# Performance work log

Hardware: AMD Instinct MI355X
Metric: run time of the kernel (lower is better)

The kernel has to match this reference:

```python
import jax, jax.numpy as jnp
import numpy as np

E, V, F_, B = 8192, 2048, 2048, 8
H, DEC, EDGE, META = 128, 128, 2, 4
MEMH, MEMAGG, AGGH = 256, 128, 128
IN_DIM = DEC + EDGE + META  # 134


def _incidence(idx, n):
    # dense (n, E) 0/1 incidence matrix, as used by torch.mm in the original
    return jnp.zeros((n, idx.shape[0]), jnp.float32).at[idx, jnp.arange(idx.shape[0])].set(1.0)


def setup_inputs() -> dict:
    key = jax.random.key(0)
    ks = jax.random.split(key, 32)
    var_idx = jax.random.randint(ks[0], (E,), 0, V)          # variable of each edge
    fun_idx = jax.random.randint(ks[1], (E,), 0, F_)         # clause of each edge
    batch_of_var = jax.random.randint(ks[2], (V,), 0, B)     # problem id of each variable
    variable_mask = _incidence(var_idx, V)                   # (V, E)
    function_mask = _incidence(fun_idx, F_)                  # (F, E)
    b_variable_mask = jnp.zeros((V, B), jnp.float32).at[jnp.arange(V), batch_of_var].set(1.0)

    def lin(k, i, o):
        kw, kb = jax.random.split(k)
        return (jax.random.normal(kw, (i, o), jnp.float32) * 0.05,
                jax.random.normal(kb, (o,), jnp.float32) * 0.05)

    p = {}
    for pre, k0 in (("v", 10), ("f", 20)):
        p[pre + "M1w"], p[pre + "M1b"] = lin(ks[k0], IN_DIM, MEMH)
        p[pre + "M2w"], p[pre + "M2b"] = lin(ks[k0 + 1], MEMH, MEMAGG)
        p[pre + "A1w"], p[pre + "A1b"] = lin(ks[k0 + 2], MEMAGG + EDGE, AGGH)
        p[pre + "A2w"], p[pre + "A2b"] = lin(ks[k0 + 3], AGGH, H)

    return dict(
        variable_state=jax.random.normal(ks[3], (E, H), jnp.float32),
        function_state=jax.random.normal(ks[4], (E, H), jnp.float32),
        decimator_variable_state=jax.random.normal(ks[5], (E, DEC), jnp.float32),
        decimator_function_state=jax.random.normal(ks[6], (E, DEC), jnp.float32),
        edge_feature=jax.random.normal(ks[7], (E, EDGE), jnp.float32),
        meta_data=jax.random.normal(ks[8], (B, META), jnp.float32),
        active_mask=jax.random.randint(ks[9], (B, 1), 0, 2),
        variable_mask=variable_mask, variable_mask_t=variable_mask.T,
        function_mask=function_mask, function_mask_t=function_mask.T,
        b_variable_mask=b_variable_mask,
        **p,
    )


def _aggregate(state, feature, mask, mask_t, W1, b1, W2, b2, A1, c1, A2, c2):
    # MessageAggregator (include_self_message=False, edge_mask=None)
    h = jax.nn.relu(state @ W1 + b1)       # (E, MEMH)  pre-aggregation transform
    h = h @ W2 + b2                        # (E, MEMAGG)
    agg = mask_t @ (mask @ h) - h          # node-sum broadcast back to edges, minus self message
    a = jax.nn.relu(jnp.concatenate([agg, feature], 1) @ A1 + c1)  # post-agg transform
    return a @ A2 + c2                     # (E, H)


def reference(variable_state, function_state, decimator_variable_state,
              decimator_function_state, edge_feature, meta_data, active_mask,
              variable_mask, variable_mask_t, function_mask, function_mask_t,
              b_variable_mask,
              vM1w, vM1b, vM2w, vM2b, vA1w, vA1b, vA2w, vA2b,
              fM1w, fM1b, fM2w, fM2b, fA1w, fA1b, fA2w, fA2b):
    # active mask broadcast: batch -> variables -> edges (dense mm chain as in torch)
    mask = variable_mask_t @ (b_variable_mask @ active_mask.astype(jnp.float32))  # (E, 1)
    # meta-data broadcast: batch -> variables -> edges
    graph_feat = variable_mask_t @ (b_variable_mask @ meta_data)                  # (E, META)

    dvs = jnp.concatenate([decimator_variable_state, edge_feature, graph_feat], 1)
    agg_v = _aggregate(dvs, edge_feature, variable_mask, variable_mask_t,
                       vM1w, vM1b, vM2w, vM2b, vA1w, vA1b, vA2w, vA2b)
    function_state = mask * agg_v + (1.0 - mask) * function_state  # dropout: identity (eval)

    dfs = jnp.concatenate([decimator_function_state, edge_feature, graph_feat], 1)
    agg_f = _aggregate(dfs, edge_feature, function_mask, function_mask_t,
                       fM1w, fM1b, fM2w, fM2b, fA1w, fA1b, fA2w, fA2b)
    variable_state = mask * agg_f + (1.0 - mask) * variable_state

    return (variable_state, function_state)
```

## Files before the change

kernel.cpp:

```cpp
#include <hip/hip_runtime.h>

#define E_N 8192
#define V_N 2048
#define F_N 2048
#define B_N 8
#define H_N 128
#define DEC_N 128
#define EDGE_N 2
#define META_N 4
#define IN_DIM 134
#define MEMH 256
#define MEMAGG 128
#define AGGH 128

typedef __attribute__((ext_vector_type(8))) short short8;
typedef __attribute__((ext_vector_type(4))) float f32x4;

__device__ inline unsigned short f2bf(float x) {
    unsigned u = __float_as_uint(x);
    unsigned r = (u + 0x7FFFu + ((u >> 16) & 1u)) >> 16;
    return (unsigned short)r;
}

__device__ inline short8 pack8(float4 u0, float4 u1) {
    short8 s;
    s[0] = (short)f2bf(u0.x); s[1] = (short)f2bf(u0.y);
    s[2] = (short)f2bf(u0.z); s[3] = (short)f2bf(u0.w);
    s[4] = (short)f2bf(u1.x); s[5] = (short)f2bf(u1.y);
    s[6] = (short)f2bf(u1.z); s[7] = (short)f2bf(u1.w);
    return s;
}

struct RDesc { const float* src; unsigned short* dst; int K; int N; int Kp; };
struct SetupArgs { RDesc d[8]; float* nszero; const float* bvm; int* bov; };

__global__ __launch_bounds__(256) void k_setup(SetupArgs p) {
    if (blockIdx.y == 8) {
        if (blockIdx.x < 8) {
            int v = blockIdx.x * 256 + threadIdx.x;
            float s = 0.f;
#pragma unroll
            for (int b = 0; b < B_N; ++b) s += p.bvm[v * B_N + b] * (float)b;
            p.bov[v] = (int)(s + 0.5f);
        }
        return;
    }
    int gid = (int)((blockIdx.y * 160 + blockIdx.x) * 256 + threadIdx.x);
    const int NZ4 = (V_N + F_N) * MEMAGG / 4;
    if (gid < NZ4) ((float4*)p.nszero)[gid] = (float4){0.f, 0.f, 0.f, 0.f};

    RDesc d = p.d[blockIdx.y];
    int i = blockIdx.x * 256 + threadIdx.x;
    int total = d.Kp * d.N;
    if (i >= total) return;
    int elem = i & 7;
    int lane = (i >> 3) & 63;
    int f    = i >> 9;
    int c16n = d.N >> 4;
    int c16 = f % c16n, kc = f / c16n;
    int k = kc * 32 + (lane >> 4) * 8 + elem;
    int c = c16 * 16 + (lane & 15);
    float v = (k < d.K) ? d.src[(size_t)k * d.N + c] : 0.f;
    d.dst[i] = f2bf(v);
}

__global__ __launch_bounds__(256) void k_idx(const float* __restrict__ vmt,
                                             const float* __restrict__ fmt,
                                             int* __restrict__ vidx,
                                             int* __restrict__ fidx,
                                             const int* __restrict__ bov,
                                             const int* __restrict__ active,
                                             const float* __restrict__ meta,
                                             float* __restrict__ emask,
                                             float* __restrict__ gfeat) {
    int wave = (int)((blockIdx.x * blockDim.x + threadIdx.x) >> 6);
    int lane = threadIdx.x & 63;
    bool isVar = wave < E_N;
    const float* m = isVar ? vmt : fmt;
    int* out = isVar ? vidx : fidx;
    int e = isVar ? wave : wave - E_N;
    const float4* row = (const float4*)(m + (size_t)e * V_N);

    int pos = -1;
#pragma unroll
    for (int half = 0; half < 2; ++half) {
        if (pos < 0) {
            float4 v0 = row[half * 256 + lane];
            float4 v1 = row[half * 256 + 64 + lane];
            float4 v2 = row[half * 256 + 128 + lane];
            float4 v3 = row[half * 256 + 192 + lane];
            int hit = -1;
            float4 vv[4] = {v0, v1, v2, v3};
#pragma unroll
            for (int j = 0; j < 4; ++j) {
                float4 v = vv[j];
                int c = (half * 256 + j * 64 + lane) * 4;
                if (hit < 0) {
                    if      (v.x != 0.f) hit = c;
                    else if (v.y != 0.f) hit = c + 1;
                    else if (v.z != 0.f) hit = c + 2;
                    else if (v.w != 0.f) hit = c + 3;
                }
            }
            unsigned long long bm = __ballot(hit >= 0);
            if (bm) pos = __shfl(hit, __ffsll((long long)bm) - 1);
        }
    }
    if (lane == 0) {
        out[e] = pos;
        if (isVar) {
            int b = bov[pos];
            emask[e] = (float)active[b];
            ((float4*)gfeat)[e] = ((const float4*)meta)[b];
        }
    }
}

struct F1Args {
    const float* dec[2];
    const float* ef;
    const float* gfeat;
    const unsigned short* wpack[2];
    const float* b1[2];
    const float* b2[2];
    const int* idx[2];
    float* h2[2];
    float* ns[2];
};

__global__ __launch_bounds__(256) void k_fused1(F1Args A) {
    int br = blockIdx.y;
    const float* dec = A.dec[br];
    const unsigned short* W1f = A.wpack[br];
    const unsigned short* W2f = A.wpack[br] + 160 * 256;
    const float* b1 = A.b1[br];
    const float* b2 = A.b2[br];
    const int* idx = A.idx[br];
    float* h2o = A.h2[br];
    float* ns  = A.ns[br];

    int tid = threadIdx.x;
    int wave = tid >> 6, lane = tid & 63;
    int lrow = lane & 15, lgrp = lane >> 4;
    int e0 = blockIdx.x * 16;

    __shared__ unsigned short h1s[16 * 256];

    int n0 = wave * 64;
    f32x4 acc1[4];
#pragma unroll
    for (int nt = 0; nt < 4; ++nt) {
        float bv = b1[n0 + nt * 16 + lrow];
        acc1[nt] = (f32x4){bv, bv, bv, bv};
    }
    const float4* dec4 = (const float4*)dec;
    int r = e0 + lrow;
#pragma unroll
    for (int kc = 0; kc < 5; ++kc) {
        short8 a;
        if (kc < 4) {
            float4 u0 = dec4[(size_t)r * 32 + kc * 8 + lgrp * 2];
            float4 u1 = dec4[(size_t)r * 32 + kc * 8 + lgrp * 2 + 1];
            a = pack8(u0, u1);
        } else {
            short8 z = (short8)0;
            if (lgrp == 0) {
                z[0] = (short)f2bf(A.ef[r * 2]);
                z[1] = (short)f2bf(A.ef[r * 2 + 1]);
                z[2] = (short)f2bf(A.gfeat[r * 4]);
                z[3] = (short)f2bf(A.gfeat[r * 4 + 1]);
                z[4] = (short)f2bf(A.gfeat[r * 4 + 2]);
                z[5] = (short)f2bf(A.gfeat[r * 4 + 3]);
            }
            a = z;
        }
#pragma unroll
        for (int nt = 0; nt < 4; ++nt) {
            short8 b = *(const short8*)(W1f + ((size_t)(kc * 16 + (n0 >> 4) + nt) * 64 + lane) * 8);
            acc1[nt] = __builtin_amdgcn_mfma_f32_16x16x32_bf16(a, b, acc1[nt], 0, 0, 0);
        }
    }
#pragma unroll
    for (int nt = 0; nt < 4; ++nt)
#pragma unroll
        for (int j = 0; j < 4; ++j) {
            int row = lgrp * 4 + j;
            int col = n0 + nt * 16 + lrow;
            h1s[row * 256 + (col ^ ((row & 7) << 3))] = f2bf(fmaxf(acc1[nt][j], 0.f));
        }
    __syncthreads();

    int c0 = wave * 32;
    f32x4 acc2[2];
#pragma unroll
    for (int nt = 0; nt < 2; ++nt) {
        float bv = b2[c0 + nt * 16 + lrow];
        acc2[nt] = (f32x4){bv, bv, bv, bv};
    }
#pragma unroll
    for (int kc = 0; kc < 8; ++kc) {
        int kb = kc * 32 + lgrp * 8;
        short8 a2 = *(const short8*)(h1s + lrow * 256 + (kb ^ ((lrow & 7) << 3)));
#pragma unroll
        for (int nt = 0; nt < 2; ++nt) {
            short8 b = *(const short8*)(W2f + ((size_t)(kc * 8 + (c0 >> 4) + nt) * 64 + lane) * 8);
            acc2[nt] = __builtin_amdgcn_mfma_f32_16x16x32_bf16(a2, b, acc2[nt], 0, 0, 0);
        }
    }
#pragma unroll
    for (int j = 0; j < 4; ++j) {
        int row = e0 + lgrp * 4 + j;
        int node = idx[row];
#pragma unroll
        for (int nt = 0; nt < 2; ++nt) {
            int col = c0 + nt * 16 + lrow;
            float v = acc2[nt][j];
            h2o[(size_t)row * 128 + col] = v;
            atomicAdd(ns + (size_t)node * 128 + col, v);
        }
    }
}

struct F2Args {
    const unsigned short* wpack[2];
    const float* c1[2];
    const float* c2[2];
    const float* h2[2];
    const float* ns[2];
    const int* idx[2];
    const float* ef;
    const float* emask;
    const float* oldst[2];
    float* outst[2];
};

__global__ __launch_bounds__(256) void k_fused2(F2Args A) {
    int br = blockIdx.y;
    const unsigned short* A1f = A.wpack[br] + 160 * 256 + 256 * 128;
    const unsigned short* A2f = A1f + 160 * 128;
    const float* c1 = A.c1[br];
    const float* c2 = A.c2[br];
    const float* h2 = A.h2[br];
    const float* ns = A.ns[br];
    const int* idx = A.idx[br];
    const float* oldst = A.oldst[br];
    float* outst = A.outst[br];

    int tid = threadIdx.x;
    int wave = tid >> 6, lane = tid & 63;
    int lrow = lane & 15, lgrp = lane >> 4;
    int e0 = blockIdx.x * 16;

    __shared__ unsigned short as_[16 * 128];

    int n0 = wave * 32;
    f32x4 accp[2];
#pragma unroll
    for (int nt = 0; nt < 2; ++nt) {
        float bv = c1[n0 + nt * 16 + lrow];
        accp[nt] = (f32x4){bv, bv, bv, bv};
    }
    const float4* ns4 = (const float4*)ns;
    const float4* h24 = (const float4*)h2;
    int r = e0 + lrow;
    int node = idx[r];
#pragma unroll
    for (int kc = 0; kc < 5; ++kc) {
        short8 a;
        if (kc < 4) {
            float4 u0 = ns4[(size_t)node * 32 + kc * 8 + lgrp * 2];
            float4 u1 = ns4[(size_t)node * 32 + kc * 8 + lgrp * 2 + 1];
            float4 v0 = h24[(size_t)r * 32 + kc * 8 + lgrp * 2];
            float4 v1 = h24[(size_t)r * 32 + kc * 8 + lgrp * 2 + 1];
            float4 d0 = {u0.x - v0.x, u0.y - v0.y, u0.z - v0.z, u0.w - v0.w};
            float4 d1 = {u1.x - v1.x, u1.y - v1.y, u1.z - v1.z, u1.w - v1.w};
            a = pack8(d0, d1);
        } else {
            short8 z = (short8)0;
            if (lgrp == 0) {
                z[0] = (short)f2bf(A.ef[r * 2]);
                z[1] = (short)f2bf(A.ef[r * 2 + 1]);
            }
            a = z;
        }
#pragma unroll
        for (int nt = 0; nt < 2; ++nt) {
            short8 b = *(const short8*)(A1f + ((size_t)(kc * 8 + (n0 >> 4) + nt) * 64 + lane) * 8);
            accp[nt] = __builtin_amdgcn_mfma_f32_16x16x32_bf16(a, b, accp[nt], 0, 0, 0);
        }
    }
#pragma unroll
    for (int nt = 0; nt < 2; ++nt)
#pragma unroll
        for (int j = 0; j < 4; ++j) {
            int row = lgrp * 4 + j;
            int col = n0 + nt * 16 + lrow;
            as_[row * 128 + (col ^ ((row & 7) << 3))] = f2bf(fmaxf(accp[nt][j], 0.f));
        }
    __syncthreads();

    f32x4 acco[2];
#pragma unroll
    for (int nt = 0; nt < 2; ++nt) {
        float bv = c2[n0 + nt * 16 + lrow];
        acco[nt] = (f32x4){bv, bv, bv, bv};
    }
#pragma unroll
    for (int kc = 0; kc < 4; ++kc) {
        int kb = kc * 32 + lgrp * 8;
        short8 a2 = *(const short8*)(as_ + lrow * 128 + (kb ^ ((lrow & 7) << 3)));
#pragma unroll
        for (int nt = 0; nt < 2; ++nt) {
            short8 b = *(const short8*)(A2f + ((size_t)(kc * 8 + (n0 >> 4) + nt) * 64 + lane) * 8);
            acco[nt] = __builtin_amdgcn_mfma_f32_16x16x32_bf16(a2, b, acco[nt], 0, 0, 0);
        }
    }
#pragma unroll
    for (int j = 0; j < 4; ++j) {
        int row = e0 + lgrp * 4 + j;
        float m = A.emask[row];
#pragma unroll
        for (int nt = 0; nt < 2; ++nt) {
            int col = n0 + nt * 16 + lrow;
            float old = oldst[(size_t)row * 128 + col];
            outst[(size_t)row * 128 + col] = m * acco[nt][j] + (1.f - m) * old;
        }
    }
}

extern "C" void kernel_launch(void* const* d_in, const int* in_sizes, int n_in,
                              void* d_out, int out_size, void* d_ws, size_t ws_size,
                              hipStream_t stream) {
    const float* variable_state = (const float*)d_in[0];
    const float* function_state = (const float*)d_in[1];
    const float* dec_v          = (const float*)d_in[2];
    const float* dec_f          = (const float*)d_in[3];
    const float* ef             = (const float*)d_in[4];
    const float* meta           = (const float*)d_in[5];
    const int*   active         = (const int*)d_in[6];
    const float* vmask_t        = (const float*)d_in[8];
    const float* fmask_t        = (const float*)d_in[10];
    const float* bvm            = (const float*)d_in[11];
    const float* vM1w = (const float*)d_in[12]; const float* vM1b = (const float*)d_in[13];
    const float* vM2w = (const float*)d_in[14]; const float* vM2b = (const float*)d_in[15];
    const float* vA1w = (const float*)d_in[16]; const float* vA1b = (const float*)d_in[17];
    const float* vA2w = (const float*)d_in[18]; const float* vA2b = (const float*)d_in[19];
    const float* fM1w = (const float*)d_in[20]; const float* fM1b = (const float*)d_in[21];
    const float* fM2w = (const float*)d_in[22]; const float* fM2b = (const float*)d_in[23];
    const float* fA1w = (const float*)d_in[24]; const float* fA1b = (const float*)d_in[25];
    const float* fA2w = (const float*)d_in[26]; const float* fA2b = (const float*)d_in[27];

    float* out_vs = (float*)d_out;
    float* out_fs = (float*)d_out + (size_t)E_N * H_N;

    int*   var_idx = (int*)d_ws;
    int*   fun_idx = var_idx + E_N;
    int*   bov     = fun_idx + E_N;
    float* emask   = (float*)(bov + V_N);
    float* gfeat   = emask + E_N;
    float* hv2     = gfeat + (size_t)E_N * 4;
    float* hf2     = hv2 + (size_t)E_N * MEMAGG;
    float* nsv     = hf2 + (size_t)E_N * MEMAGG;
    float* nsf     = nsv + (size_t)V_N * MEMAGG;
    unsigned short* wpack = (unsigned short*)(nsf + (size_t)F_N * MEMAGG);
    const int PBR = 160 * 256 + 256 * 128 + 160 * 128 + 128 * 128;
    unsigned short* wpv = wpack;
    unsigned short* wpf = wpack + PBR;

    SetupArgs sp;
    sp.d[0] = {vM1w, wpv,                          IN_DIM, MEMH,   160};
    sp.d[1] = {vM2w, wpv + 160 * 256,              MEMH,   MEMAGG, 256};
    sp.d[2] = {vA1w, wpv + 160 * 256 + 256 * 128,  130,    AGGH,   160};
    sp.d[3] = {vA2w, wpv + 160 * 256 + 256 * 128 + 160 * 128, 128, H_N, 128};
    sp.d[4] = {fM1w, wpf,                          IN_DIM, MEMH,   160};
    sp.d[5] = {fM2w, wpf + 160 * 256,              MEMH,   MEMAGG, 256};
    sp.d[6] = {fA1w, wpf + 160 * 256 + 256 * 128,  130,    AGGH,   160};
    sp.d[7] = {fA2w, wpf + 160 * 256 + 256 * 128 + 160 * 128, 128, H_N, 128};
    sp.nszero = nsv;
    sp.bvm = bvm;
    sp.bov = bov;
    k_setup<<<dim3(160, 9), 256, 0, stream>>>(sp);

    k_idx<<<(2 * E_N) / 4, 256, 0, stream>>>(vmask_t, fmask_t, var_idx, fun_idx,
                                             bov, active, meta, emask, gfeat);

    F1Args f1;
    f1.dec[0] = dec_v;  f1.dec[1] = dec_f;
    f1.ef = ef;         f1.gfeat = gfeat;
    f1.wpack[0] = wpv;  f1.wpack[1] = wpf;
    f1.b1[0] = vM1b;    f1.b1[1] = fM1b;
    f1.b2[0] = vM2b;    f1.b2[1] = fM2b;
    f1.idx[0] = var_idx; f1.idx[1] = fun_idx;
    f1.h2[0] = hv2;     f1.h2[1] = hf2;
    f1.ns[0] = nsv;     f1.ns[1] = nsf;
    k_fused1<<<dim3(E_N / 16, 2), 256, 0, stream>>>(f1);

    F2Args f2;
    f2.wpack[0] = wpv;  f2.wpack[1] = wpf;
    f2.c1[0] = vA1b;    f2.c1[1] = fA1b;
    f2.c2[0] = vA2b;    f2.c2[1] = fA2b;
    f2.h2[0] = hv2;     f2.h2[1] = hf2;
    f2.ns[0] = nsv;     f2.ns[1] = nsf;
    f2.idx[0] = var_idx; f2.idx[1] = fun_idx;
    f2.ef = ef;         f2.emask = emask;
    f2.oldst[0] = function_state;  f2.oldst[1] = variable_state;
    f2.outst[0] = out_fs;          f2.outst[1] = out_vs;
    k_fused2<<<dim3(E_N / 16, 2), 256, 0, stream>>>(f2);
}
```

Measured before the change: 58.37 us.

## Fuse function-mask index scan into first fused kernel and batch row scans per wave

The incidence-row scan for the function branch moves out of the standalone index kernel and into the start of the first fused MLP kernel. Found indices go to shared memory for the scatter-add and are also written to global for the later kernel. The variable-branch scan now gives each wave four rows with all first-half loads issued up front to raise memory-level parallelism. The aim is to overlap the function-mask scan with variable-side work and shorten the index kernel, at the cost of extra latency and register pressure at the start of the fused kernel.

```diff
diff --git a/kernel.cpp b/kernel.cpp
--- a/kernel.cpp
+++ b/kernel.cpp
@@ -29,6 +29,16 @@
     s[4] = (short)f2bf(u1.x); s[5] = (short)f2bf(u1.y);
     s[6] = (short)f2bf(u1.z); s[7] = (short)f2bf(u1.w);
     return s;
+}
+
+__device__ inline int probe4(float4 v, int c, int hit) {
+    if (hit < 0) {
+        if      (v.x != 0.f) hit = c;
+        else if (v.y != 0.f) hit = c + 1;
+        else if (v.z != 0.f) hit = c + 2;
+        else if (v.w != 0.f) hit = c + 3;
+    }
+    return hit;
 }
 
 struct RDesc { const float* src; unsigned short* dst; int K; int N; int Kp; };
@@ -64,54 +74,43 @@
     d.dst[i] = f2bf(v);
 }
 
-__global__ __launch_bounds__(256) void k_idx(const float* __restrict__ vmt,
-                                             const float* __restrict__ fmt,
-                                             int* __restrict__ vidx,
-                                             int* __restrict__ fidx,
-                                             const int* __restrict__ bov,
-                                             const int* __restrict__ active,
-                                             const float* __restrict__ meta,
-                                             float* __restrict__ emask,
-                                             float* __restrict__ gfeat) {
-    int wave = (int)((blockIdx.x * blockDim.x + threadIdx.x) >> 6);
-    int lane = threadIdx.x & 63;
-    bool isVar = wave < E_N;
-    const float* m = isVar ? vmt : fmt;
-    int* out = isVar ? vidx : fidx;
-    int e = isVar ? wave : wave - E_N;
-    const float4* row = (const float4*)(m + (size_t)e * V_N);
-
-    int pos = -1;
-#pragma unroll
-    for (int half = 0; half < 2; ++half) {
-        if (pos < 0) {
-            float4 v0 = row[half * 256 + lane];
-            float4 v1 = row[half * 256 + 64 + lane];
-            float4 v2 = row[half * 256 + 128 + lane];
-            float4 v3 = row[half * 256 + 192 + lane];
-            int hit = -1;
-            float4 vv[4] = {v0, v1, v2, v3};
+__global__ __launch_bounds__(256) void k_scanv(const float* __restrict__ vmt,
+                                               int* __restrict__ vidx,
+                                               const int* __restrict__ bov,
+                                               const int* __restrict__ active,
+                                               const float* __restrict__ meta,
+                                               float* __restrict__ emask,
+                                               float* __restrict__ gfeat) {
+    int wave = threadIdx.x >> 6, lane = threadIdx.x & 63;
+    int e0 = blockIdx.x * 16 + wave * 4;
+    const float4* rp[4];
+    float4 h[4][4];
+#pragma unroll
+    for (int r = 0; r < 4; ++r) {
+        rp[r] = (const float4*)(vmt + (size_t)(e0 + r) * V_N);
+#pragma unroll
+        for (int j = 0; j < 4; ++j) h[r][j] = rp[r][j * 64 + lane];
+    }
+#pragma unroll
+    for (int r = 0; r < 4; ++r) {
+        int hit = -1;
+#pragma unroll
+        for (int j = 0; j < 4; ++j) hit = probe4(h[r][j], (j * 64 + lane) * 4, hit);
+        unsigned long long bm = __ballot(hit >= 0);
+        if (!bm) {
 #pragma unroll
             for (int j = 0; j < 4; ++j) {
-                float4 v = vv[j];
-                int c = (half * 256 + j * 64 + lane) * 4;
-                if (hit < 0) {
-                    if      (v.x != 0.f) hit = c;
-                    else if (v.y != 0.f) hit = c + 1;
-                    else if (v.z != 0.f) hit = c + 2;
-                    else if (v.w != 0.f) hit = c + 3;
-                }
+                float4 v = rp[r][256 + j * 64 + lane];
+                hit = probe4(v, 1024 + (j * 64 + lane) * 4, hit);
             }
-            unsigned long long bm = __ballot(hit >= 0);
-            if (bm) pos = __shfl(hit, __ffsll((long long)bm) - 1);
-        }
-    }
-    if (lane == 0) {
-        out[e] = pos;
-        if (isVar) {
+            bm = __ballot(hit >= 0);
+        }
+        int pos = __shfl(hit, __ffsll((long long)bm) - 1);
+        if (lane == 0) {
+            vidx[e0 + r] = pos;
             int b = bov[pos];
-            emask[e] = (float)active[b];
-            ((float4*)gfeat)[e] = ((const float4*)meta)[b];
+            emask[e0 + r] = (float)active[b];
+            ((float4*)gfeat)[e0 + r] = ((const float4*)meta)[b];
         }
     }
 }
@@ -120,10 +119,11 @@
     const float* dec[2];
     const float* ef;
     const float* gfeat;
+    const float* fmt;
     const unsigned short* wpack[2];
     const float* b1[2];
     const float* b2[2];
-    const int* idx[2];
+    int* idx[2];
     float* h2[2];
     float* ns[2];
 };
@@ -135,7 +135,6 @@
     const unsigned short* W2f = A.wpack[br] + 160 * 256;
     const float* b1 = A.b1[br];
     const float* b2 = A.b2[br];
-    const int* idx = A.idx[br];
     float* h2o = A.h2[br];
     float* ns  = A.ns[br];
 
@@ -145,6 +144,41 @@
     int e0 = blockIdx.x * 16;
 
     __shared__ unsigned short h1s[16 * 256];
+    __shared__ int idxs[16];
+
+    if (br == 0) {
+        if (tid < 16) idxs[tid] = A.idx[0][e0 + tid];
+    } else {
+        int ew = e0 + wave * 4;
+        const float4* rp[4];
+        float4 h[4][4];
+#pragma unroll
+        for (int r = 0; r < 4; ++r) {
+            rp[r] = (const float4*)(A.fmt + (size_t)(ew + r) * F_N);
+#pragma unroll
+            for (int j = 0; j < 4; ++j) h[r][j] = rp[r][j * 64 + lane];
+        }
+#pragma unroll
+        for (int r = 0; r < 4; ++r) {
+            int hit = -1;
+#pragma unroll
+            for (int j = 0; j < 4; ++j) hit = probe4(h[r][j], (j * 64 + lane) * 4, hit);
+            unsigned long long bm = __ballot(hit >= 0);
+            if (!bm) {
+#pragma unroll
+                for (int j = 0; j < 4; ++j) {
+                    float4 v = rp[r][256 + j * 64 + lane];
+                    hit = probe4(v, 1024 + (j * 64 + lane) * 4, hit);
+                }
+                bm = __ballot(hit >= 0);
+            }
+            int pos = __shfl(hit, __ffsll((long long)bm) - 1);
+            if (lane == 0) {
+                idxs[wave * 4 + r] = pos;
+                A.idx[1][ew + r] = pos;
+            }
+        }
+    }
 
     int n0 = wave * 64;
     f32x4 acc1[4];
@@ -210,7 +244,7 @@
 #pragma unroll
     for (int j = 0; j < 4; ++j) {
         int row = e0 + lgrp * 4 + j;
-        int node = idx[row];
+        int node = idxs[lgrp * 4 + j];
 #pragma unroll
         for (int nt = 0; nt < 2; ++nt) {
             int col = c0 + nt * 16 + lrow;
@@ -381,12 +415,13 @@
     sp.bov = bov;
     k_setup<<<dim3(160, 9), 256, 0, stream>>>(sp);
 
-    k_idx<<<(2 * E_N) / 4, 256, 0, stream>>>(vmask_t, fmask_t, var_idx, fun_idx,
-                                             bov, active, meta, emask, gfeat);
+    k_scanv<<<E_N / 16, 256, 0, stream>>>(vmask_t, var_idx, bov, active, meta,
+                                          emask, gfeat);
 
     F1Args f1;
     f1.dec[0] = dec_v;  f1.dec[1] = dec_f;
     f1.ef = ef;         f1.gfeat = gfeat;
+    f1.fmt = fmask_t;
     f1.wpack[0] = wpv;  f1.wpack[1] = wpf;
     f1.b1[0] = vM1b;    f1.b1[1] = fM1b;
     f1.b2[0] = vM2b;    f1.b2[1] = fM2b;
```

After: 68.09 us. 1.17x slower.

## Merge setup and index-scan kernels into one prep kernel with finer-grained early-exit scan

Applied to the files above, without the earlier changes.

Combines the weight-packing/zeroing kernel and the incidence-row scan kernel into a single launch with block-range dispatch, removing one launch and its serialization. Row scanning now reads 512-float chunks with an early exit after each chunk instead of 1024-float halves, cutting wasted reads of dense incidence rows. The batch-of-variable lookup is computed inline from the batch mask, dropping the intermediate bov buffer and its dependency. Each wave handles two rows, which adds per-wave serial latency in exchange for fewer waves.

```diff
diff --git a/kernel.cpp b/kernel.cpp
--- a/kernel.cpp
+++ b/kernel.cpp
@@ -31,28 +31,83 @@
     return s;
 }
 
+__device__ inline int probe4(float4 v, int c, int hit) {
+    if (hit < 0) {
+        if      (v.x != 0.f) hit = c;
+        else if (v.y != 0.f) hit = c + 1;
+        else if (v.z != 0.f) hit = c + 2;
+        else if (v.w != 0.f) hit = c + 3;
+    }
+    return hit;
+}
+
+__device__ inline int scan_row(const float4* rp, int lane) {
+    float4 a0 = rp[lane], a1 = rp[64 + lane];
+    int hit = probe4(a0, lane * 4, -1);
+    hit = probe4(a1, (64 + lane) * 4, hit);
+    unsigned long long bm = __ballot(hit >= 0);
+    for (int base = 128; base < 512 && !bm; base += 128) {
+        float4 v0 = rp[base + lane], v1 = rp[base + 64 + lane];
+        hit = probe4(v0, (base + lane) * 4, hit);
+        hit = probe4(v1, (base + 64 + lane) * 4, hit);
+        bm = __ballot(hit >= 0);
+    }
+    return __shfl(hit, __ffsll((long long)bm) - 1);
+}
+
 struct RDesc { const float* src; unsigned short* dst; int K; int N; int Kp; };
-struct SetupArgs { RDesc d[8]; float* nszero; const float* bvm; int* bov; };
-
-__global__ __launch_bounds__(256) void k_setup(SetupArgs p) {
-    if (blockIdx.y == 8) {
-        if (blockIdx.x < 8) {
-            int v = blockIdx.x * 256 + threadIdx.x;
-            float s = 0.f;
-#pragma unroll
-            for (int b = 0; b < B_N; ++b) s += p.bvm[v * B_N + b] * (float)b;
-            p.bov[v] = (int)(s + 0.5f);
+struct PrepArgs {
+    const float* vmt; const float* fmt;
+    int* vidx; int* fidx;
+    const float* bvm; const int* active; const float* meta;
+    float* emask; float* gfeat;
+    float* nszero;
+    RDesc d[8];
+};
+__constant__ const int RP_CUM[9] = {0, 160, 288, 368, 432, 592, 720, 800, 864};
+
+__global__ __launch_bounds__(256) void k_prep(PrepArgs P) {
+    int bid = blockIdx.x, tid = threadIdx.x;
+    if (bid < 2048) {
+        int wave = bid * 4 + (tid >> 6);
+        int lane = tid & 63;
+        int r0 = wave * 2;
+        bool isVar = r0 < E_N;
+        const float* m = isVar ? P.vmt : P.fmt;
+        int* out = isVar ? P.vidx : P.fidx;
+        int e0 = isVar ? r0 : r0 - E_N;
+        const float4* rpA = (const float4*)(m + (size_t)e0 * V_N);
+        const float4* rpB = (const float4*)(m + (size_t)(e0 + 1) * V_N);
+        int posA = scan_row(rpA, lane);
+        int posB = scan_row(rpB, lane);
+        if (lane < 2) {
+            int pos = (lane == 0) ? posA : posB;
+            int e = e0 + lane;
+            out[e] = pos;
+            if (isVar) {
+                const float4* bv = (const float4*)(P.bvm + pos * 8);
+                float4 x0 = bv[0], x1 = bv[1];
+                float s = x0.y + 2.f * x0.z + 3.f * x0.w +
+                          4.f * x1.x + 5.f * x1.y + 6.f * x1.z + 7.f * x1.w;
+                int b = (int)(s + 0.5f);
+                P.emask[e] = (float)P.active[b];
+                ((float4*)P.gfeat)[e] = ((const float4*)P.meta)[b];
+            }
         }
         return;
     }
-    int gid = (int)((blockIdx.y * 160 + blockIdx.x) * 256 + threadIdx.x);
-    const int NZ4 = (V_N + F_N) * MEMAGG / 4;
-    if (gid < NZ4) ((float4*)p.nszero)[gid] = (float4){0.f, 0.f, 0.f, 0.f};
-
-    RDesc d = p.d[blockIdx.y];
-    int i = blockIdx.x * 256 + threadIdx.x;
-    int total = d.Kp * d.N;
-    if (i >= total) return;
+    if (bid < 2560) {
+        int gid = (bid - 2048) * 256 + tid;
+        ((float4*)P.nszero)[gid] = (float4){0.f, 0.f, 0.f, 0.f};
+        return;
+    }
+    int rb = bid - 2560;
+    int mi = 0;
+#pragma unroll
+    for (int t = 1; t < 8; ++t) if (rb >= RP_CUM[t]) mi = t;
+    RDesc d = P.d[mi];
+    int i = (rb - RP_CUM[mi]) * 256 + tid;
+    if (i >= d.Kp * d.N) return;
     int elem = i & 7;
     int lane = (i >> 3) & 63;
     int f    = i >> 9;
@@ -62,58 +117,6 @@
     int c = c16 * 16 + (lane & 15);
     float v = (k < d.K) ? d.src[(size_t)k * d.N + c] : 0.f;
     d.dst[i] = f2bf(v);
-}
-
-__global__ __launch_bounds__(256) void k_idx(const float* __restrict__ vmt,
-                                             const float* __restrict__ fmt,
-                                             int* __restrict__ vidx,
-                                             int* __restrict__ fidx,
-                                             const int* __restrict__ bov,
-                                             const int* __restrict__ active,
-                                             const float* __restrict__ meta,
-                                             float* __restrict__ emask,
-                                             float* __restrict__ gfeat) {
-    int wave = (int)((blockIdx.x * blockDim.x + threadIdx.x) >> 6);
-    int lane = threadIdx.x & 63;
-    bool isVar = wave < E_N;
-    const float* m = isVar ? vmt : fmt;
-    int* out = isVar ? vidx : fidx;
-    int e = isVar ? wave : wave - E_N;
-    const float4* row = (const float4*)(m + (size_t)e * V_N);
-
-    int pos = -1;
-#pragma unroll
-    for (int half = 0; half < 2; ++half) {
-        if (pos < 0) {
-            float4 v0 = row[half * 256 + lane];
-            float4 v1 = row[half * 256 + 64 + lane];
-            float4 v2 = row[half * 256 + 128 + lane];
-            float4 v3 = row[half * 256 + 192 + lane];
-            int hit = -1;
-            float4 vv[4] = {v0, v1, v2, v3};
-#pragma unroll
-            for (int j = 0; j < 4; ++j) {
-                float4 v = vv[j];
-                int c = (half * 256 + j * 64 + lane) * 4;
-                if (hit < 0) {
-                    if      (v.x != 0.f) hit = c;
-                    else if (v.y != 0.f) hit = c + 1;
-                    else if (v.z != 0.f) hit = c + 2;
-                    else if (v.w != 0.f) hit = c + 3;
-                }
-            }
-            unsigned long long bm = __ballot(hit >= 0);
-            if (bm) pos = __shfl(hit, __ffsll((long long)bm) - 1);
-        }
-    }
-    if (lane == 0) {
-        out[e] = pos;
-        if (isVar) {
-            int b = bov[pos];
-            emask[e] = (float)active[b];
-            ((float4*)gfeat)[e] = ((const float4*)meta)[b];
-        }
-    }
 }
 
 struct F1Args {
@@ -355,8 +358,7 @@
 
     int*   var_idx = (int*)d_ws;
     int*   fun_idx = var_idx + E_N;
-    int*   bov     = fun_idx + E_N;
-    float* emask   = (float*)(bov + V_N);
+    float* emask   = (float*)(fun_idx + E_N);
     float* gfeat   = emask + E_N;
     float* hv2     = gfeat + (size_t)E_N * 4;
     float* hf2     = hv2 + (size_t)E_N * MEMAGG;
@@ -367,22 +369,21 @@
     unsigned short* wpv = wpack;
     unsigned short* wpf = wpack + PBR;
 
-    SetupArgs sp;
-    sp.d[0] = {vM1w, wpv,                          IN_DIM, MEMH,   160};
-    sp.d[1] = {vM2w, wpv + 160 * 256,              MEMH,   MEMAGG, 256};
-    sp.d[2] = {vA1w, wpv + 160 * 256 + 256 * 128,  130,    AGGH,   160};
-    sp.d[3] = {vA2w, wpv + 160 * 256 + 256 * 128 + 160 * 128, 128, H_N, 128};
-    sp.d[4] = {fM1w, wpf,                          IN_DIM, MEMH,   160};
-    sp.d[5] = {fM2w, wpf + 160 * 256,              MEMH,   MEMAGG, 256};
-    sp.d[6] = {fA1w, wpf + 160 * 256 + 256 * 128,  130,    AGGH,   160};
-    sp.d[7] = {fA2w, wpf + 160 * 256 + 256 * 128 + 160 * 128, 128, H_N, 128};
-    sp.nszero = nsv;
-    sp.bvm = bvm;
-    sp.bov = bov;
-    k_setup<<<dim3(160, 9), 256, 0, stream>>>(sp);
-
-    k_idx<<<(2 * E_N) / 4, 256, 0, stream>>>(vmask_t, fmask_t, var_idx, fun_idx,
-                                             bov, active, meta, emask, gfeat);
+    PrepArgs pp;
+    pp.vmt = vmask_t; pp.fmt = fmask_t;
+    pp.vidx = var_idx; pp.fidx = fun_idx;
+    pp.bvm = bvm; pp.active = active; pp.meta = meta;
+    pp.emask = emask; pp.gfeat = gfeat;
+    pp.nszero = nsv;
+    pp.d[0] = {vM1w, wpv,                          IN_DIM, MEMH,   160};
+    pp.d[1] = {vM2w, wpv + 160 * 256,              MEMH,   MEMAGG, 256};
+    pp.d[2] = {vA1w, wpv + 160 * 256 + 256 * 128,  130,    AGGH,   160};
+    pp.d[3] = {vA2w, wpv + 160 * 256 + 256 * 128 + 160 * 128, 128, H_N, 128};
+    pp.d[4] = {fM1w, wpf,                          IN_DIM, MEMH,   160};
+    pp.d[5] = {fM2w, wpf + 160 * 256,              MEMH,   MEMAGG, 256};
+    pp.d[6] = {fA1w, wpf + 160 * 256 + 256 * 128,  130,    AGGH,   160};
+    pp.d[7] = {fA2w, wpf + 160 * 256 + 256 * 128 + 160 * 128, 128, H_N, 128};
+    k_prep<<<3424, 256, 0, stream>>>(pp);
 
     F1Args f1;
     f1.dec[0] = dec_v;  f1.dec[1] = dec_f;
```

Result: faster. 52.89 us (-9.4%).
